# Kernel optimization log

Hardware: AMD Instinct MI355X
Metric: run time of the kernel (lower is better)

The kernel has to match this reference:

```python
import jax, jax.numpy as jnp
import numpy as np
from jax import lax

N, C_IN, DIMS, NW, T, H, W = 8, 64, 64, 8, 16, 64, 64
BN_EPS = 1e-5


def setup_inputs() -> dict:
    key = jax.random.key(0)
    ks = jax.random.split(key, 10)
    # kaiming-ish scales
    w_scale = (2.0 / (C_IN * 27)) ** 0.5
    return {
        "x": jax.random.normal(ks[0], (N, C_IN, T, H, W), dtype=jnp.float32),
        "weights": jax.random.normal(ks[1], (NW, DIMS, C_IN, 3, 3, 3), dtype=jnp.float32) * w_scale,
        "biases": jax.random.normal(ks[2], (NW, DIMS), dtype=jnp.float32),
        "se_w1": jax.random.normal(ks[3], (16, C_IN, 5, 5), dtype=jnp.float32) * (2.0 / (C_IN * 25)) ** 0.5,
        "se_b1": jnp.zeros((16,), dtype=jnp.float32),
        "se_w2": jax.random.normal(ks[4], (32, 16, 5, 5), dtype=jnp.float32) * (2.0 / (16 * 25)) ** 0.5,
        "se_b2": jnp.zeros((32,), dtype=jnp.float32),
        "lin_w": jax.random.normal(ks[5], (NW, 32), dtype=jnp.float32) * (1.0 / 32) ** 0.5,
        "lin_b": jnp.zeros((NW,), dtype=jnp.float32),
        "bn_gamma": jnp.ones((DIMS,), dtype=jnp.float32),
        "bn_beta": jnp.zeros((DIMS,), dtype=jnp.float32),
        "epochs_num": 15,
    }


def _forward(x, weights, biases, se_w1, se_b1, se_w2, se_b2, lin_w, lin_b, bn_gamma, bn_beta, epochs_num):
    tau = 30.0 - 2.9 * epochs_num if epochs_num < 10 else 1.0
    # std over temporal axis (torch.std -> unbiased, ddof=1): [n, c, h, w]
    std_x = jnp.std(x, axis=2, ddof=1)
    # squeeze-expand attention branch
    dn2d = ("NCHW", "OIHW", "NCHW")
    h1 = lax.conv_general_dilated(std_x, se_w1, (1, 1), "VALID", dimension_numbers=dn2d)
    h1 = jax.nn.relu(h1 + se_b1[None, :, None, None])
    h2 = lax.conv_general_dilated(h1, se_w2, (1, 1), "VALID", dimension_numbers=dn2d)
    h2 = jax.nn.relu(h2 + se_b2[None, :, None, None])
    pooled = jnp.max(h2, axis=(2, 3))                      # [n, 32]
    logits = pooled @ lin_w.T + lin_b                       # [n, num_weights]
    phi = jax.nn.softmax(logits / tau, axis=1)
    # per-sample dynamic kernels / biases
    dyn_w = jnp.einsum("bn,ncidhw->bcidhw", phi, weights)   # [n, dims, c_in, 3,3,3]
    dyn_b = phi @ biases                                    # [n, dims]
    # grouped conv3d (groups = n) == per-sample conv3d via vmap
    dn3d = ("NCDHW", "OIDHW", "NCDHW")
    def one_conv(xi, wi):
        return lax.conv_general_dilated(xi[None], wi, (1, 1, 1), "SAME", dimension_numbers=dn3d)[0]
    y = jax.vmap(one_conv)(x, dyn_w)                        # [n, dims, t, h, w]
    y = y + dyn_b[:, :, None, None, None]
    # BatchNorm3d (training mode, batch stats, biased var)
    mean = jnp.mean(y, axis=(0, 2, 3, 4))
    var = jnp.var(y, axis=(0, 2, 3, 4))
    b = lambda v: v[None, :, None, None, None]
    y = (y - b(mean)) * b(bn_gamma) * lax.rsqrt(b(var) + BN_EPS) + b(bn_beta)
    return jax.nn.relu(y)


def reference(x, weights, biases, se_w1, se_b1, se_w2, se_b2, lin_w, lin_b, bn_gamma, bn_beta, epochs_num):
    return _forward(x, weights, biases, se_w1, se_b1, se_w2, se_b2, lin_w, lin_b, bn_gamma, bn_beta, epochs_num)
```

## Files before the change

kernel.cpp:

```cpp
#include <hip/hip_runtime.h>
#include <hip/hip_bf16.h>
#include <math.h>

#define N_   8
#define CIN_ 64
#define DIMS_ 64
#define NW_  8
#define T_   16
#define H_   64
#define W_   64
#define HW_  (H_ * W_)
#define THW_ (T_ * HW_)

typedef short bf16x8 __attribute__((ext_vector_type(8)));
typedef float f32x16 __attribute__((ext_vector_type(16)));

__device__ __forceinline__ unsigned short f2bf(float f) {
    union { float f; unsigned u; } a; a.f = f;
    unsigned r = a.u + 0x7fffu + ((a.u >> 16) & 1u);
    return (unsigned short)(r >> 16);
}

#define CS8_ 8
#define HS8_ (66 * CS8_)
#define TS8_ (10 * HS8_)
#define XSH_ (3 * TS8_)
#define WLH_ (28 * 64 * 8)

__host__ __device__ constexpr int OXc(int tap) {
    int tt = tap > 26 ? 26 : tap;
    return (tt / 9) * TS8_ + ((tt % 9) / 3) * HS8_ + ((tt % 3) - 1) * CS8_;
}

__global__ __launch_bounds__(512) void stdxb_kernel(
    const float* __restrict__ x, float* __restrict__ std_x,
    unsigned short* __restrict__ xb, float* __restrict__ sums,
    unsigned* __restrict__ pooled)
{
    __shared__ unsigned short xsl[16 * 64 * 8];
    const int h = blockIdx.x, c8 = blockIdx.y, n = blockIdx.z;
    const int tid = threadIdx.x;
    if ((blockIdx.x | blockIdx.y | blockIdx.z) == 0) {
        if (tid < 128) sums[tid] = 0.f;
        else if (tid < 384) pooled[tid - 128] = 0u;
    }
    const int c = tid >> 6, w = tid & 63;
    const int cin = c8 * 8 + c;
    const float* px = x + (((size_t)(n * 64 + cin)) << 16) + (h << 6) + w;
    float s = 0.f, s2 = 0.f;
#pragma unroll
    for (int t = 0; t < T_; ++t) {
        float v = px[t * HW_];
        s += v;
        s2 += v * v;
        xsl[(t << 9) + (w << 3) + c] = f2bf(v);
    }
    float var = (s2 - s * s * (1.0f / 16.0f)) * (1.0f / 15.0f);
    std_x[(((size_t)(n * 64 + cin)) << 12) + (h << 6) + w] = sqrtf(fmaxf(var, 0.f));
    __syncthreads();
    const int4* src = (const int4*)xsl;
    int4* dst = (int4*)(xb + ((size_t)((n * 8 + c8) * 16) << 12) * 8);
#pragma unroll
    for (int k = 0; k < 2; ++k) {
        int j = tid + (k << 9);
        int t = j >> 6, ww = j & 63;
        dst[((t << 6) + h) * 64 + ww] = src[j];
    }
}

__global__ void wtrans(const float* __restrict__ w1, const float* __restrict__ w2,
                       float* __restrict__ w1t, float* __restrict__ w2t) {
    int i = blockIdx.x * 256 + threadIdx.x;
    if (i < 25600) {
        int k = i / 1600, c = (i / 25) % 64, tap = i % 25;
        w1t[(c * 25 + tap) * 16 + k] = w1[i];
    } else if (i < 38400) {
        int j = i - 25600;
        int o = j / 400, c = (j / 25) % 16, tap = j % 25;
        w2t[(c * 25 + tap) * 32 + o] = w2[j];
    }
}

__global__ __launch_bounds__(256) void se_conv1c(const float* __restrict__ std_x,
        const float* __restrict__ w1t, const float* __restrict__ b1, float* __restrict__ h1) {
    __shared__ float red[3][64][8];
    const int n = blockIdx.y, ks = blockIdx.z * 8;
    const int iq = threadIdx.x & 63, cq = threadIdx.x >> 6;
    const int ij = blockIdx.x * 64 + iq;
    float acc[8];
#pragma unroll
    for (int q = 0; q < 8; ++q) acc[q] = 0.f;
    if (ij < 3600) {
        int i = ij / 60, j = ij - i * 60;
        const float* xn = std_x + (size_t)n * CIN_ * HW_ + i * W_ + j;
        for (int c = cq * 16; c < cq * 16 + 16; ++c) {
            const float* xc = xn + c * HW_;
            float xv[25];
#pragma unroll
            for (int u = 0; u < 5; ++u)
#pragma unroll
                for (int v = 0; v < 5; ++v) xv[u * 5 + v] = xc[u * W_ + v];
            const float* wc = w1t + c * 400 + ks;
#pragma unroll
            for (int tap = 0; tap < 25; ++tap)
#pragma unroll
                for (int q = 0; q < 8; ++q)
                    acc[q] = fmaf(xv[tap], wc[tap * 16 + q], acc[q]);
        }
    }
    if (cq > 0) {
#pragma unroll
        for (int q = 0; q < 8; ++q) red[cq - 1][iq][q] = acc[q];
    }
    __syncthreads();
    if (cq == 0 && ij < 3600) {
#pragma unroll
        for (int q = 0; q < 8; ++q) {
            float a = acc[q] + red[0][iq][q] + red[1][iq][q] + red[2][iq][q] + b1[ks + q];
            h1[((size_t)(n * 16 + ks + q)) * 3600 + ij] = fmaxf(a, 0.f);
        }
    }
}

__global__ __launch_bounds__(256) void se_conv2c(const float* __restrict__ h1,
        const float* __restrict__ w2t, const float* __restrict__ b2,
        unsigned* __restrict__ pooled) {
    __shared__ float red[3][64][8];
    const int n = blockIdx.y, os = blockIdx.z * 8;
    const int iq = threadIdx.x & 63, cq = threadIdx.x >> 6;
    const int ij = blockIdx.x * 64 + iq;
    const int i = ij / 56, j = ij - i * 56;
    float acc[8];
#pragma unroll
    for (int q = 0; q < 8; ++q) acc[q] = 0.f;
    const float* xn = h1 + (size_t)n * 16 * 3600 + i * 60 + j;
    for (int c = cq * 4; c < cq * 4 + 4; ++c) {
        const float* xc = xn + c * 3600;
        float xv[25];
#pragma unroll
        for (int u = 0; u < 5; ++u)
#pragma unroll
            for (int v = 0; v < 5; ++v) xv[u * 5 + v] = xc[u * 60 + v];
        const float* wc = w2t + c * 800 + os;
#pragma unroll
        for (int tap = 0; tap < 25; ++tap)
#pragma unroll
            for (int q = 0; q < 8; ++q)
                acc[q] = fmaf(xv[tap], wc[tap * 32 + q], acc[q]);
    }
    if (cq > 0) {
#pragma unroll
        for (int q = 0; q < 8; ++q) red[cq - 1][iq][q] = acc[q];
    }
    __syncthreads();
    if (cq == 0) {
#pragma unroll
        for (int q = 0; q < 8; ++q) {
            float a = fmaxf(acc[q] + red[0][iq][q] + red[1][iq][q] + red[2][iq][q] + b2[os + q], 0.f);
#pragma unroll
            for (int m = 1; m < 64; m <<= 1) a = fmaxf(a, __shfl_xor(a, m, 64));
            if (iq == 0) atomicMax(&pooled[n * 32 + os + q], __float_as_uint(a));
        }
    }
}

__global__ __launch_bounds__(256) void dyn_w_head(
    const float* __restrict__ weights, const float* __restrict__ pooled,
    const float* __restrict__ lin_w, const float* __restrict__ lin_b,
    const float* __restrict__ biases, const int* __restrict__ epochs,
    unsigned short* __restrict__ wtb2, float* __restrict__ dyn_b) {
    __shared__ float slog[8][8];
    __shared__ float sphi[64];
    const int tid = threadIdx.x;
    const int e = epochs[0];
    const float tau = (e < 10) ? (30.0f - 2.9f * (float)e) : 1.0f;
    if (tid < 64) {
        int b = tid >> 3, m = tid & 7;
        float acc = lin_b[m];
#pragma unroll
        for (int k = 0; k < 32; ++k) acc += pooled[b * 32 + k] * lin_w[m * 32 + k];
        slog[b][m] = acc / tau;
    }
    __syncthreads();
    if (tid < 8) {
        float mx = slog[tid][0];
#pragma unroll
        for (int m = 1; m < 8; ++m) mx = fmaxf(mx, slog[tid][m]);
        float ex[8], ssum = 0.f;
#pragma unroll
        for (int m = 0; m < 8; ++m) { ex[m] = expf(slog[tid][m] - mx); ssum += ex[m]; }
        float inv = 1.0f / ssum;
#pragma unroll
        for (int m = 0; m < 8; ++m) sphi[tid * 8 + m] = ex[m] * inv;
    }
    __syncthreads();
    if (blockIdx.x < 64) {
        int b = blockIdx.x >> 3, c8 = blockIdx.x & 7;
        unsigned* dst = (unsigned*)(wtb2 + (size_t)b * 114688 + (size_t)(c8 * 28 + 27) * 512);
        dst[tid] = 0u;
    }
    if (blockIdx.x == 0) {
#pragma unroll
        for (int idx = tid; idx < 512; idx += 256) {
            int b = idx >> 6, d = idx & 63;
            float a = 0.f;
#pragma unroll
            for (int m = 0; m < 8; ++m) a += sphi[b * 8 + m] * biases[m * DIMS_ + d];
            dyn_b[idx] = a;
        }
    }
    int f = blockIdx.x * 256 + tid;
    if (f >= 110592) return;
    int tap = f % 27, cin = (f / 27) & 63, co = f / 1728;
    float wv[8];
#pragma unroll
    for (int m = 0; m < 8; ++m) wv[m] = weights[(size_t)m * 110592 + f];
    size_t dbase = (size_t)(cin >> 3) * 14336 + tap * 512 + co * 8 + (cin & 7);
#pragma unroll
    for (int b = 0; b < 8; ++b) {
        float acc = 0.f;
#pragma unroll
        for (int m = 0; m < 8; ++m) acc += sphi[b * 8 + m] * wv[m];
        wtb2[(size_t)b * 114688 + dbase] = f2bf(acc);
    }
}

__global__ __launch_bounds__(256, 2) void conv3d_mfma5(
    const unsigned short* __restrict__ xb,
    const unsigned short* __restrict__ wtb2,
    const float* __restrict__ dynb,
    float* __restrict__ y,
    float* __restrict__ sums)
{
    __shared__ __align__(16) unsigned short xs[XSH_];
    __shared__ __align__(16) unsigned short wl[WLH_];
    __shared__ float bnred[128];

    const int hb = blockIdx.x, t = blockIdx.y, n = blockIdx.z;
    const int tid = threadIdx.x;
    const int lane = tid & 63, wid = tid >> 6;
    const int lane31 = lane & 31, tau = lane >> 5;
    const int hbase = hb * 8;

    for (int i = tid; i < XSH_ / 8; i += 256)
        *(int4*)&xs[i * 8] = (int4){0, 0, 0, 0};
    if (tid < 128) bnred[tid] = 0.f;

    const unsigned short* xnb = xb + (size_t)n * 4194304;
    const unsigned short* wnb = wtb2 + (size_t)n * 114688;

    f32x16 acc[2][4];
#pragma unroll
    for (int ci = 0; ci < 2; ++ci)
#pragma unroll
        for (int s = 0; s < 4; ++s)
            acc[ci][s] = (f32x16)(0.f);

    const int aBase = tau * 512 + lane31 * 8;
    int bsp[4];
#pragma unroll
    for (int s = 0; s < 4; ++s)
        bsp[s] = (2 * wid + (s >> 1)) * HS8_ + (1 + (s & 1) * 32 + lane31) * CS8_;

    for (int c8 = 0; c8 < 8; ++c8) {
        __syncthreads();
#pragma unroll
        for (int k = 0; k < 7; ++k) {
            int tp = wid + (k << 2);
            const unsigned short* gp = wnb + ((size_t)c8 * 14336 + tp * 512 + lane * 8);
            const unsigned short* lp = &wl[tp * 512];
            __builtin_amdgcn_global_load_lds(
                (const __attribute__((address_space(1))) void*)gp,
                (__attribute__((address_space(3))) void*)lp, 16, 0, 0);
        }
#pragma unroll
        for (int k = 0; k < 8; ++k) {
            int r = wid + (k << 2);
            if (r < 30) {
                int tp = (r >= 20) ? 2 : (r >= 10 ? 1 : 0);
                int hp = r - tp * 10;
                int gt = t + tp - 1, gh = hbase + hp - 1;
                if (((unsigned)gt < 16u) && ((unsigned)gh < 64u)) {
                    const unsigned short* gp = xnb + (size_t)(((c8 * 16 + gt) * 64 + gh) * 64 + lane) * 8;
                    const unsigned short* lp = &xs[tp * TS8_ + hp * HS8_ + CS8_];
                    __builtin_amdgcn_global_load_lds(
                        (const __attribute__((address_space(1))) void*)gp,
                        (__attribute__((address_space(3))) void*)lp, 16, 0, 0);
                }
            }
        }
        __syncthreads();

#pragma unroll
        for (int p = 0; p < 14; ++p) {
            const int xo = tau ? OXc(2 * p + 1) : OXc(2 * p);
            bf16x8 a0 = *(const bf16x8*)&wl[p * 1024 + aBase];
            bf16x8 a1 = *(const bf16x8*)&wl[p * 1024 + aBase + 256];
            bf16x8 b0 = *(const bf16x8*)&xs[bsp[0] + xo];
            bf16x8 b1 = *(const bf16x8*)&xs[bsp[1] + xo];
            bf16x8 b2 = *(const bf16x8*)&xs[bsp[2] + xo];
            bf16x8 b3 = *(const bf16x8*)&xs[bsp[3] + xo];
            acc[0][0] = __builtin_amdgcn_mfma_f32_32x32x16_bf16(a0, b0, acc[0][0], 0, 0, 0);
            acc[0][1] = __builtin_amdgcn_mfma_f32_32x32x16_bf16(a0, b1, acc[0][1], 0, 0, 0);
            acc[0][2] = __builtin_amdgcn_mfma_f32_32x32x16_bf16(a0, b2, acc[0][2], 0, 0, 0);
            acc[0][3] = __builtin_amdgcn_mfma_f32_32x32x16_bf16(a0, b3, acc[0][3], 0, 0, 0);
            acc[1][0] = __builtin_amdgcn_mfma_f32_32x32x16_bf16(a1, b0, acc[1][0], 0, 0, 0);
            acc[1][1] = __builtin_amdgcn_mfma_f32_32x32x16_bf16(a1, b1, acc[1][1], 0, 0, 0);
            acc[1][2] = __builtin_amdgcn_mfma_f32_32x32x16_bf16(a1, b2, acc[1][2], 0, 0, 0);
            acc[1][3] = __builtin_amdgcn_mfma_f32_32x32x16_bf16(a1, b3, acc[1][3], 0, 0, 0);
        }
    }

    const float* db = dynb + n * DIMS_;
#pragma unroll
    for (int ci = 0; ci < 2; ++ci) {
#pragma unroll
        for (int r = 0; r < 16; ++r) {
            const int co = 32 * ci + (r & 3) + 8 * (r >> 2) + 4 * tau;
            const float bco = db[co];
            float ps = 0.f, ps2 = 0.f;
#pragma unroll
            for (int s = 0; s < 4; ++s) {
                float z = acc[ci][s][r] + bco;
                size_t yi = ((size_t)(n * 64 + co) << 16) + ((size_t)t << 12)
                          + ((size_t)(hbase + 2 * wid + (s >> 1)) << 6) + (s & 1) * 32 + lane31;
                y[yi] = z;
                ps += z;
                ps2 += z * z;
            }
#pragma unroll
            for (int m = 1; m < 32; m <<= 1) {
                ps += __shfl_xor(ps, m, 64);
                ps2 += __shfl_xor(ps2, m, 64);
            }
            if (lane31 == 0) {
                atomicAdd(&bnred[co], ps);
                atomicAdd(&bnred[64 + co], ps2);
            }
        }
    }
    __syncthreads();
    if (tid < 128) atomicAdd(&sums[tid], bnred[tid]);
}

__global__ void bn_norm4(const float* __restrict__ sums, const float* __restrict__ gamma,
                         const float* __restrict__ beta, float* __restrict__ y) {
    const float cnt = (float)(N_ * THW_);
    for (size_t idx = (size_t)blockIdx.x * 256 + threadIdx.x; idx < 8388608;
         idx += (size_t)4096 * 256) {
        int c = (int)((idx >> 14) & 63);
        float mean = sums[c] / cnt;
        float var = sums[64 + c] / cnt - mean * mean;
        float sc = gamma[c] * rsqrtf(var + 1e-5f);
        float sh = beta[c] - mean * sc;
        float4 v = ((float4*)y)[idx];
        v.x = fmaxf(fmaf(v.x, sc, sh), 0.f);
        v.y = fmaxf(fmaf(v.y, sc, sh), 0.f);
        v.z = fmaxf(fmaf(v.z, sc, sh), 0.f);
        v.w = fmaxf(fmaf(v.w, sc, sh), 0.f);
        ((float4*)y)[idx] = v;
    }
}

extern "C" void kernel_launch(void* const* d_in, const int* in_sizes, int n_in,
                              void* d_out, int out_size, void* d_ws, size_t ws_size,
                              hipStream_t stream) {
    const float* x       = (const float*)d_in[0];
    const float* weights = (const float*)d_in[1];
    const float* biases  = (const float*)d_in[2];
    const float* se_w1   = (const float*)d_in[3];
    const float* se_b1   = (const float*)d_in[4];
    const float* se_w2   = (const float*)d_in[5];
    const float* se_b2   = (const float*)d_in[6];
    const float* lin_w   = (const float*)d_in[7];
    const float* lin_b   = (const float*)d_in[8];
    const float* gamma   = (const float*)d_in[9];
    const float* beta    = (const float*)d_in[10];
    const int*   epochs  = (const int*)d_in[11];

    float* out = (float*)d_out;
    float* ws = (float*)d_ws;

    const size_t STD_OFF  = 0;
    const size_t H1_OFF   = STD_OFF + 2097152;
    const size_t SUMS_OFF = H1_OFF + 460800;
    const size_t POOL_OFF = SUMS_OFF + 128;
    const size_t PHI_OFF  = POOL_OFF + 256;
    const size_t DYNB_OFF = PHI_OFF + 64;
    const size_t WTB_OFF  = DYNB_OFF + 512;
    const size_t W1T_OFF  = WTB_OFF + 458752;
    const size_t W2T_OFF  = W1T_OFF + 25600;
    const size_t XB_OFF   = W2T_OFF + 12800;

    float* std_x  = ws + STD_OFF;
    float* h1     = ws + H1_OFF;
    float* sums   = ws + SUMS_OFF;
    float* pooled = ws + POOL_OFF;
    float* dynb   = ws + DYNB_OFF;
    unsigned short* wtb2 = (unsigned short*)(ws + WTB_OFF);
    float* w1t    = ws + W1T_OFF;
    float* w2t    = ws + W2T_OFF;
    unsigned short* xb = (unsigned short*)(ws + XB_OFF);

    stdxb_kernel<<<dim3(64, 8, 8), 512, 0, stream>>>(x, std_x, xb, sums, (unsigned*)pooled);
    wtrans<<<150, 256, 0, stream>>>(se_w1, se_w2, w1t, w2t);

    se_conv1c<<<dim3(57, 8, 2), 256, 0, stream>>>(std_x, w1t, se_b1, h1);
    se_conv2c<<<dim3(49, 8, 4), 256, 0, stream>>>(h1, w2t, se_b2, (unsigned*)pooled);

    dyn_w_head<<<432, 256, 0, stream>>>(weights, pooled, lin_w, lin_b, biases, epochs,
                                        wtb2, dynb);

    conv3d_mfma5<<<dim3(8, 16, 8), 256, 0, stream>>>(xb, wtb2, dynb, out, sums);

    bn_norm4<<<4096, 256, 0, stream>>>(sums, gamma, beta, out);
}
```

Measured before the change: 372.2 us.

## Double-buffer conv3d LDS staging with 1024-thread blocks covering two time slices

The conv3d kernel is rebuilt as 1024-thread blocks that each compute two output time slices. Input halo and weight tiles go through a double-buffered dynamic LDS region, and the next channel group is prefetched asynchronously while the current one feeds the MFMA loop. Loads that fall outside the volume are redirected to a junk LDS slot, so every thread issues a uniform count that the explicit vmcnt waits rely on. The small SE weight-transpose kernel is folded into the std/bf16 conversion kernel to save a launch. The trade-off is roughly 144KB of LDS per block, which likely limits occupancy to one block per CU, and a grid that shrinks to 512 blocks.

```diff
diff --git a/kernel.cpp b/kernel.cpp
--- a/kernel.cpp
+++ b/kernel.cpp
@@ -24,8 +24,15 @@
 #define CS8_ 8
 #define HS8_ (66 * CS8_)
 #define TS8_ (10 * HS8_)
-#define XSH_ (3 * TS8_)
-#define WLH_ (28 * 64 * 8)
+#define XB4_ (4 * TS8_)
+#define WB_  (28 * 64 * 8)
+#define XOFF0_ 0
+#define XOFF1_ XB4_
+#define WOFF0_ (2 * XB4_)
+#define WOFF1_ (2 * XB4_ + WB_)
+#define JUNK_  (2 * XB4_ + 2 * WB_)
+#define BNRED_ (JUNK_ + 512)
+#define DLS_BYTES_ ((BNRED_ + 256) * 2)
 
 __host__ __device__ constexpr int OXc(int tap) {
     int tt = tap > 26 ? 26 : tap;
@@ -35,14 +42,28 @@
 __global__ __launch_bounds__(512) void stdxb_kernel(
     const float* __restrict__ x, float* __restrict__ std_x,
     unsigned short* __restrict__ xb, float* __restrict__ sums,
-    unsigned* __restrict__ pooled)
+    unsigned* __restrict__ pooled,
+    const float* __restrict__ w1, const float* __restrict__ w2,
+    float* __restrict__ w1t, float* __restrict__ w2t)
 {
     __shared__ unsigned short xsl[16 * 64 * 8];
     const int h = blockIdx.x, c8 = blockIdx.y, n = blockIdx.z;
     const int tid = threadIdx.x;
-    if ((blockIdx.x | blockIdx.y | blockIdx.z) == 0) {
+    const int bf = blockIdx.x + (blockIdx.y << 6) + ((int)blockIdx.z << 9);
+    if (bf == 0) {
         if (tid < 128) sums[tid] = 0.f;
         else if (tid < 384) pooled[tid - 128] = 0u;
+    }
+    if (bf < 75) {
+        int i = bf * 512 + tid;
+        if (i < 25600) {
+            int k = i / 1600, c = (i / 25) % 64, tap = i % 25;
+            w1t[(c * 25 + tap) * 16 + k] = w1[i];
+        } else if (i < 38400) {
+            int j = i - 25600;
+            int o = j / 400, c = (j / 25) % 16, tap = j % 25;
+            w2t[(c * 25 + tap) * 32 + o] = w2[j];
+        }
     }
     const int c = tid >> 6, w = tid & 63;
     const int cin = c8 * 8 + c;
@@ -65,19 +86,6 @@
         int j = tid + (k << 9);
         int t = j >> 6, ww = j & 63;
         dst[((t << 6) + h) * 64 + ww] = src[j];
-    }
-}
-
-__global__ void wtrans(const float* __restrict__ w1, const float* __restrict__ w2,
-                       float* __restrict__ w1t, float* __restrict__ w2t) {
-    int i = blockIdx.x * 256 + threadIdx.x;
-    if (i < 25600) {
-        int k = i / 1600, c = (i / 25) % 64, tap = i % 25;
-        w1t[(c * 25 + tap) * 16 + k] = w1[i];
-    } else if (i < 38400) {
-        int j = i - 25600;
-        int o = j / 400, c = (j / 25) % 16, tap = j % 25;
-        w2t[(c * 25 + tap) * 32 + o] = w2[j];
     }
 }
 
@@ -225,109 +233,117 @@
     }
 }
 
-__global__ __launch_bounds__(256, 2) void conv3d_mfma5(
+extern __shared__ unsigned short dls[];
+
+__global__ __launch_bounds__(1024, 4) void conv3d_mfma6(
     const unsigned short* __restrict__ xb,
     const unsigned short* __restrict__ wtb2,
     const float* __restrict__ dynb,
     float* __restrict__ y,
     float* __restrict__ sums)
 {
-    __shared__ __align__(16) unsigned short xs[XSH_];
-    __shared__ __align__(16) unsigned short wl[WLH_];
-    __shared__ float bnred[128];
-
-    const int hb = blockIdx.x, t = blockIdx.y, n = blockIdx.z;
+    const int hb = blockIdx.x, tp2 = blockIdx.y, n = blockIdx.z;
     const int tid = threadIdx.x;
     const int lane = tid & 63, wid = tid >> 6;
     const int lane31 = lane & 31, tau = lane >> 5;
-    const int hbase = hb * 8;
-
-    for (int i = tid; i < XSH_ / 8; i += 256)
-        *(int4*)&xs[i * 8] = (int4){0, 0, 0, 0};
+    const int t_loc = wid >> 3, hrow = wid & 7;
+    const int hbase = hb * 8, t2 = tp2 * 2;
+
+    float* bnred = (float*)(dls + BNRED_);
+
+    for (int i = tid; i < (2 * XB4_) / 8; i += 1024)
+        *(int4*)&dls[i * 8] = (int4){0, 0, 0, 0};
     if (tid < 128) bnred[tid] = 0.f;
+    __syncthreads();
 
     const unsigned short* xnb = xb + (size_t)n * 4194304;
     const unsigned short* wnb = wtb2 + (size_t)n * 114688;
 
-    f32x16 acc[2][4];
-#pragma unroll
-    for (int ci = 0; ci < 2; ++ci)
-#pragma unroll
-        for (int s = 0; s < 4; ++s)
-            acc[ci][s] = (f32x16)(0.f);
-
-    const int aBase = tau * 512 + lane31 * 8;
-    int bsp[4];
-#pragma unroll
-    for (int s = 0; s < 4; ++s)
-        bsp[s] = (2 * wid + (s >> 1)) * HS8_ + (1 + (s & 1) * 32 + lane31) * CS8_;
-
-    for (int c8 = 0; c8 < 8; ++c8) {
-        __syncthreads();
-#pragma unroll
-        for (int k = 0; k < 7; ++k) {
-            int tp = wid + (k << 2);
-            const unsigned short* gp = wnb + ((size_t)c8 * 14336 + tp * 512 + lane * 8);
-            const unsigned short* lp = &wl[tp * 512];
+    auto STAGE = [&](int c8, int pb) {
+        unsigned short* xbuf = dls + (pb ? XOFF1_ : XOFF0_);
+        unsigned short* wbuf = dls + (pb ? WOFF1_ : WOFF0_);
+        unsigned short* junk = dls + JUNK_;
+#pragma unroll
+        for (int k = 0; k < 5; ++k) {
+            int u = wid + (k << 4);
+            const unsigned short* gp;
+            unsigned short* lp;
+            if (u < 28) {
+                gp = wnb + ((size_t)c8 * 14336 + u * 512 + lane * 8);
+                lp = wbuf + u * 512;
+            } else if (u < 68) {
+                int v = u - 28;
+                int tp = v / 10, hp = v - tp * 10;
+                int gt = t2 + tp - 1, gh = hbase + hp - 1;
+                bool ok = ((unsigned)gt < 16u) && ((unsigned)gh < 64u);
+                gp = xnb + (ok ? (size_t)(((c8 * 16 + gt) * 64 + gh) * 512 + lane * 8)
+                               : (size_t)(lane * 8));
+                lp = ok ? (xbuf + tp * TS8_ + hp * HS8_ + CS8_) : junk;
+            } else {
+                gp = wnb + lane * 8;
+                lp = junk;
+            }
             __builtin_amdgcn_global_load_lds(
                 (const __attribute__((address_space(1))) void*)gp,
                 (__attribute__((address_space(3))) void*)lp, 16, 0, 0);
         }
-#pragma unroll
-        for (int k = 0; k < 8; ++k) {
-            int r = wid + (k << 2);
-            if (r < 30) {
-                int tp = (r >= 20) ? 2 : (r >= 10 ? 1 : 0);
-                int hp = r - tp * 10;
-                int gt = t + tp - 1, gh = hbase + hp - 1;
-                if (((unsigned)gt < 16u) && ((unsigned)gh < 64u)) {
-                    const unsigned short* gp = xnb + (size_t)(((c8 * 16 + gt) * 64 + gh) * 64 + lane) * 8;
-                    const unsigned short* lp = &xs[tp * TS8_ + hp * HS8_ + CS8_];
-                    __builtin_amdgcn_global_load_lds(
-                        (const __attribute__((address_space(1))) void*)gp,
-                        (__attribute__((address_space(3))) void*)lp, 16, 0, 0);
-                }
-            }
-        }
-        __syncthreads();
-
+    };
+
+    f32x16 acc[2][2];
+#pragma unroll
+    for (int ci = 0; ci < 2; ++ci)
+#pragma unroll
+        for (int s = 0; s < 2; ++s)
+            acc[ci][s] = (f32x16)(0.f);
+
+    const int aBase = tau * 512 + lane31 * 8;
+    const int bsp0 = t_loc * TS8_ + hrow * HS8_ + (1 + lane31) * CS8_;
+    const int bsp1 = bsp0 + 32 * CS8_;
+
+    STAGE(0, 0);
+
+    for (int c8 = 0; c8 < 8; ++c8) {
+        if (c8 < 7) {
+            STAGE(c8 + 1, (c8 + 1) & 1);
+            asm volatile("s_waitcnt vmcnt(5)" ::: "memory");
+        } else {
+            asm volatile("s_waitcnt vmcnt(0)" ::: "memory");
+        }
+        __builtin_amdgcn_sched_barrier(0);
+        __builtin_amdgcn_s_barrier();
+        __builtin_amdgcn_sched_barrier(0);
+
+        const unsigned short* xsb = dls + ((c8 & 1) ? XOFF1_ : XOFF0_);
+        const unsigned short* wlb = dls + ((c8 & 1) ? WOFF1_ : WOFF0_);
 #pragma unroll
         for (int p = 0; p < 14; ++p) {
             const int xo = tau ? OXc(2 * p + 1) : OXc(2 * p);
-            bf16x8 a0 = *(const bf16x8*)&wl[p * 1024 + aBase];
-            bf16x8 a1 = *(const bf16x8*)&wl[p * 1024 + aBase + 256];
-            bf16x8 b0 = *(const bf16x8*)&xs[bsp[0] + xo];
-            bf16x8 b1 = *(const bf16x8*)&xs[bsp[1] + xo];
-            bf16x8 b2 = *(const bf16x8*)&xs[bsp[2] + xo];
-            bf16x8 b3 = *(const bf16x8*)&xs[bsp[3] + xo];
+            bf16x8 a0 = *(const bf16x8*)&wlb[p * 1024 + aBase];
+            bf16x8 a1 = *(const bf16x8*)&wlb[p * 1024 + aBase + 256];
+            bf16x8 b0 = *(const bf16x8*)&xsb[bsp0 + xo];
+            bf16x8 b1 = *(const bf16x8*)&xsb[bsp1 + xo];
             acc[0][0] = __builtin_amdgcn_mfma_f32_32x32x16_bf16(a0, b0, acc[0][0], 0, 0, 0);
             acc[0][1] = __builtin_amdgcn_mfma_f32_32x32x16_bf16(a0, b1, acc[0][1], 0, 0, 0);
-            acc[0][2] = __builtin_amdgcn_mfma_f32_32x32x16_bf16(a0, b2, acc[0][2], 0, 0, 0);
-            acc[0][3] = __builtin_amdgcn_mfma_f32_32x32x16_bf16(a0, b3, acc[0][3], 0, 0, 0);
             acc[1][0] = __builtin_amdgcn_mfma_f32_32x32x16_bf16(a1, b0, acc[1][0], 0, 0, 0);
             acc[1][1] = __builtin_amdgcn_mfma_f32_32x32x16_bf16(a1, b1, acc[1][1], 0, 0, 0);
-            acc[1][2] = __builtin_amdgcn_mfma_f32_32x32x16_bf16(a1, b2, acc[1][2], 0, 0, 0);
-            acc[1][3] = __builtin_amdgcn_mfma_f32_32x32x16_bf16(a1, b3, acc[1][3], 0, 0, 0);
-        }
+        }
+        __builtin_amdgcn_s_barrier();
     }
 
     const float* db = dynb + n * DIMS_;
+    const int t_out = t2 + t_loc, h_out = hbase + hrow;
+    const size_t ybase = (((size_t)(n * 64)) << 16) + ((size_t)t_out << 12) + ((size_t)h_out << 6);
 #pragma unroll
     for (int ci = 0; ci < 2; ++ci) {
 #pragma unroll
         for (int r = 0; r < 16; ++r) {
             const int co = 32 * ci + (r & 3) + 8 * (r >> 2) + 4 * tau;
             const float bco = db[co];
-            float ps = 0.f, ps2 = 0.f;
-#pragma unroll
-            for (int s = 0; s < 4; ++s) {
-                float z = acc[ci][s][r] + bco;
-                size_t yi = ((size_t)(n * 64 + co) << 16) + ((size_t)t << 12)
-                          + ((size_t)(hbase + 2 * wid + (s >> 1)) << 6) + (s & 1) * 32 + lane31;
-                y[yi] = z;
-                ps += z;
-                ps2 += z * z;
-            }
+            float z0 = acc[ci][0][r] + bco;
+            float z1 = acc[ci][1][r] + bco;
+            y[ybase + ((size_t)co << 16) + lane31]      = z0;
+            y[ybase + ((size_t)co << 16) + 32 + lane31] = z1;
+            float ps = z0 + z1, ps2 = z0 * z0 + z1 * z1;
 #pragma unroll
             for (int m = 1; m < 32; m <<= 1) {
                 ps += __shfl_xor(ps, m, 64);
@@ -402,8 +418,11 @@
     float* w2t    = ws + W2T_OFF;
     unsigned short* xb = (unsigned short*)(ws + XB_OFF);
 
-    stdxb_kernel<<<dim3(64, 8, 8), 512, 0, stream>>>(x, std_x, xb, sums, (unsigned*)pooled);
-    wtrans<<<150, 256, 0, stream>>>(se_w1, se_w2, w1t, w2t);
+    hipFuncSetAttribute((const void*)conv3d_mfma6,
+                        hipFuncAttributeMaxDynamicSharedMemorySize, DLS_BYTES_);
+
+    stdxb_kernel<<<dim3(64, 8, 8), 512, 0, stream>>>(
+        x, std_x, xb, sums, (unsigned*)pooled, se_w1, se_w2, w1t, w2t);
 
     se_conv1c<<<dim3(57, 8, 2), 256, 0, stream>>>(std_x, w1t, se_b1, h1);
     se_conv2c<<<dim3(49, 8, 4), 256, 0, stream>>>(h1, w2t, se_b2, (unsigned*)pooled);
@@ -411,7 +430,7 @@
     dyn_w_head<<<432, 256, 0, stream>>>(weights, pooled, lin_w, lin_b, biases, epochs,
                                         wtb2, dynb);
 
-    conv3d_mfma5<<<dim3(8, 16, 8), 256, 0, stream>>>(xb, wtb2, dynb, out, sums);
+    conv3d_mfma6<<<dim3(8, 8, 8), 1024, DLS_BYTES_, stream>>>(xb, wtb2, dynb, out, sums);
 
     bn_norm4<<<4096, 256, 0, stream>>>(sums, gamma, beta, out);
 }
```

Result: no change. 377.5 us (+1.4%).
